# Kernel tuning notes

Measured on AMD Instinct MI355X. Metric: run time of the kernel, lower is better.

The kernel has to match this reference:

```python
import jax, jax.numpy as jnp
import numpy as np

NEG = -1000000.0  # mask fill value used by original sequence_mask

def setup_inputs() -> dict:
    key = jax.random.key(0)
    k1, k2, k3, k4 = jax.random.split(key, 4)
    B, S, D = 32, 2048, 64
    queries = jax.random.normal(k1, (B, S, D), dtype=jnp.float32)
    keys = jax.random.normal(k2, (B, S, D), dtype=jnp.float32)
    values = jax.random.normal(k3, (B, S, D), dtype=jnp.float32)
    valid_lens = jax.random.randint(k4, (B,), 1, S + 1, dtype=jnp.int64)
    return {"queries": queries, "keys": keys, "values": values, "valid_lens": valid_lens}

def reference(queries, keys, values, valid_lens):
    d = queries.shape[-1]
    # [B, Sq, Sk]
    scores = jnp.einsum('bqd,bkd->bqk', queries, keys) / jnp.sqrt(jnp.asarray(d, queries.dtype))
    # valid_lens is 1D: one length per batch row, broadcast over all query rows
    kv_idx = jnp.arange(scores.shape[-1])  # [Sk]
    mask = kv_idx[None, None, :] < valid_lens[:, None, None]  # [B,1,Sk] broadcast
    scores = jnp.where(mask, scores, jnp.asarray(NEG, scores.dtype))
    weights = jax.nn.softmax(scores, axis=-1)
    # dropout p=0.0 -> identity
    return jnp.einsum('bqk,bkd->bqd', weights, values)
```

## Files before the change

### kernel.cpp

```cpp
#include <hip/hip_runtime.h>
#include <hip/hip_bf16.h>

typedef __attribute__((ext_vector_type(8))) short bf16x8;
typedef __attribute__((ext_vector_type(4))) float f32x4;

#define BATCH 32
#define SEQ   2048
#define KSTR  72
#define VSTR  36
#define PSTR  20
#define LOG2E 1.44269504088896340736f

__device__ __forceinline__ unsigned int pk2(float lo, float hi) {
    __hip_bfloat162 h2 = __float22bfloat162_rn(make_float2(lo, hi));
    return *reinterpret_cast<unsigned int*>(&h2);
}

__global__ void prep_vl(const int* __restrict__ VL, int* __restrict__ meta) {
    __shared__ int sv[BATCH];
    const int t = threadIdx.x;
    int odd = (t < 16) ? VL[2 * t + 1] : 0;
    const bool is64 = (__ballot(odd != 0) == 0ULL);
    if (t < BATCH) {
        int x = is64 ? VL[2 * t] : VL[t];
        x = x < 0 ? 0 : (x > SEQ ? SEQ : x);
        sv[t] = x;
    }
    __syncthreads();
    if (t < BATCH) {
        const int x = sv[t];
        int rank = 0;
        for (int j = 0; j < BATCH; ++j) {
            const int y = sv[j];
            rank += (y > x) || (y == x && j < t);
        }
        meta[rank] = x;
        meta[BATCH + rank] = t;
    }
}

__device__ __forceinline__ void load_tile(const float* __restrict__ Kb,
                                          const float* __restrict__ Vb,
                                          int tid, f32x4 kv[4], f32x4 vv[4]) {
    #pragma unroll
    for (int h = 0; h < 4; ++h) {
        const int c = tid + h * 256;
        kv[h] = *(const f32x4*)(Kb + (c >> 4) * 64 + (c & 15) * 4);
    }
    #pragma unroll
    for (int h = 0; h < 2; ++h) {
        const int u  = tid + h * 256;
        const int d4 = (u & 3) + ((u >> 7) << 2);
        const int kp = (u >> 2) & 31;
        vv[2 * h]     = *(const f32x4*)(Vb + (2 * kp) * 64 + d4 * 4);
        vv[2 * h + 1] = *(const f32x4*)(Vb + (2 * kp + 1) * 64 + d4 * 4);
    }
}

__global__ __launch_bounds__(256, 4)
void attn_fwd(const float* __restrict__ Qp, const float* __restrict__ Kp,
              const float* __restrict__ Vp, const int* __restrict__ meta,
              float* __restrict__ Out) {
    constexpr int D = 64;
    constexpr int S = SEQ;
    constexpr int qtiles = S >> 6;
    __shared__ short        lK [64 * KSTR];
    __shared__ unsigned int lVt[64 * VSTR];
    __shared__ unsigned int lPt[4 * 32 * PSTR];

    const int tid  = threadIdx.x;
    const int wave = tid >> 6;
    const int lane = tid & 63;
    const int l15  = lane & 15;
    const int grp  = lane >> 4;

    const int slot  = blockIdx.x / qtiles;
    const int qt    = blockIdx.x % qtiles;
    const int vl    = meta[slot];
    const int batch = meta[BATCH + slot];
    const int ntiles = (vl + 63) >> 6;

    const float* Kb = Kp + (size_t)batch * S * D;
    const float* Vb = Vp + (size_t)batch * S * D;

    bf16x8 qf[2];
    {
        const float* qb = Qp + ((size_t)batch * S + qt * 64 + wave * 16 + l15) * D + grp * 8;
        #pragma unroll
        for (int kf = 0; kf < 2; ++kf) {
            union { f32x4 f; float e[4]; } a, b;
            a.f = *(const f32x4*)(qb + kf * 32);
            b.f = *(const f32x4*)(qb + kf * 32 + 4);
            union { bf16x8 v; unsigned int u[4]; } qq;
            qq.u[0] = pk2(a.e[0], a.e[1]); qq.u[1] = pk2(a.e[2], a.e[3]);
            qq.u[2] = pk2(b.e[0], b.e[1]); qq.u[3] = pk2(b.e[2], b.e[3]);
            qf[kf] = qq.v;
        }
    }

    f32x4 o[4] = {{0.f,0.f,0.f,0.f},{0.f,0.f,0.f,0.f},{0.f,0.f,0.f,0.f},{0.f,0.f,0.f,0.f}};
    float mrun = -INFINITY;
    float lrun = 0.f;
    unsigned int* pw = &lPt[wave * 32 * PSTR];

    f32x4 kv[4], vv[4];
    if (ntiles > 0) load_tile(Kb, Vb, tid, kv, vv);

    for (int kt = 0; kt < ntiles; ++kt) {
        const int kb = kt * 64;
        __syncthreads();

        #pragma unroll
        for (int h = 0; h < 4; ++h) {
            const int c = tid + h * 256;
            const int row = c >> 4, col = (c & 15) * 4;
            union { f32x4 f; float e[4]; } x; x.f = kv[h];
            unsigned int w0 = pk2(x.e[0], x.e[1]), w1 = pk2(x.e[2], x.e[3]);
            unsigned int* dst = (unsigned int*)&lK[row * KSTR + col];
            dst[0] = w0; dst[1] = w1;
        }
        #pragma unroll
        for (int h = 0; h < 2; ++h) {
            const int u  = tid + h * 256;
            const int d4 = (u & 3) + ((u >> 7) << 2);
            const int kp = (u >> 2) & 31;
            union { f32x4 f; float e[4]; } a, b;
            a.f = vv[2 * h]; b.f = vv[2 * h + 1];
            #pragma unroll
            for (int j = 0; j < 4; ++j)
                lVt[(d4 * 4 + j) * VSTR + kp] = pk2(a.e[j], b.e[j]);
        }
        if (kt + 1 < ntiles) load_tile(Kb + (size_t)(kb + 64) * D, Vb + (size_t)(kb + 64) * D, tid, kv, vv);
        __syncthreads();

        f32x4 st[4] = {{0.f,0.f,0.f,0.f},{0.f,0.f,0.f,0.f},{0.f,0.f,0.f,0.f},{0.f,0.f,0.f,0.f}};
        #pragma unroll
        for (int kf = 0; kf < 2; ++kf) {
            #pragma unroll
            for (int ct = 0; ct < 4; ++ct) {
                bf16x8 kfr = *(const bf16x8*)&lK[(ct * 16 + l15) * KSTR + kf * 32 + grp * 8];
                st[ct] = __builtin_amdgcn_mfma_f32_16x16x32_bf16(kfr, qf[kf], st[ct], 0, 0, 0);
            }
        }

        #pragma unroll
        for (int ct = 0; ct < 4; ++ct)
            #pragma unroll
            for (int r = 0; r < 4; ++r) {
                const bool valid = (kb + ct * 16 + grp * 4 + r) < vl;
                st[ct][r] = valid ? st[ct][r] * (0.125f * LOG2E) : (-1000000.0f * LOG2E);
            }

        float t0 = fmaxf(fmaxf(st[0][0], st[0][1]), fmaxf(st[0][2], st[0][3]));
        float t1 = fmaxf(fmaxf(st[1][0], st[1][1]), fmaxf(st[1][2], st[1][3]));
        float t2 = fmaxf(fmaxf(st[2][0], st[2][1]), fmaxf(st[2][2], st[2][3]));
        float t3 = fmaxf(fmaxf(st[3][0], st[3][1]), fmaxf(st[3][2], st[3][3]));
        float tm = fmaxf(fmaxf(t0, t1), fmaxf(t2, t3));
        tm = fmaxf(tm, __shfl_xor(tm, 16));
        tm = fmaxf(tm, __shfl_xor(tm, 32));
        const float mnew  = fmaxf(mrun, tm);
        const float alpha = exp2f(mrun - mnew);
        mrun = mnew;
        lrun *= alpha;
        #pragma unroll
        for (int dt = 0; dt < 4; ++dt)
            #pragma unroll
            for (int r = 0; r < 4; ++r) o[dt][r] *= alpha;

        float rs = 0.f;
        #pragma unroll
        for (int ct = 0; ct < 4; ++ct) {
            #pragma unroll
            for (int r = 0; r < 4; ++r) {
                st[ct][r] = exp2f(st[ct][r] - mrun);
                rs += st[ct][r];
            }
            #pragma unroll
            for (int a = 0; a < 2; ++a)
                pw[(ct * 8 + grp * 2 + a) * PSTR + l15] = pk2(st[ct][2 * a], st[ct][2 * a + 1]);
        }
        rs += __shfl_xor(rs, 16);
        rs += __shfl_xor(rs, 32);
        lrun += rs;
        asm volatile("s_waitcnt lgkmcnt(0)" ::: "memory");

        #pragma unroll
        for (int kk = 0; kk < 2; ++kk) {
            union { bf16x8 v; unsigned int u[4]; } pf;
            #pragma unroll
            for (int jj = 0; jj < 4; ++jj)
                pf.u[jj] = pw[(kk * 16 + grp * 4 + jj) * PSTR + l15];
            #pragma unroll
            for (int dt = 0; dt < 4; ++dt) {
                bf16x8 vf = *(const bf16x8*)&lVt[(dt * 16 + l15) * VSTR + kk * 16 + grp * 4];
                o[dt] = __builtin_amdgcn_mfma_f32_16x16x32_bf16(vf, pf.v, o[dt], 0, 0, 0);
            }
        }
    }

    const float inv = (lrun > 0.f) ? 1.0f / lrun : 0.f;
    const size_t orow = ((size_t)batch * S + qt * 64 + wave * 16 + l15) * D;
    #pragma unroll
    for (int dt = 0; dt < 4; ++dt) {
        f32x4 w = o[dt];
        w[0] *= inv; w[1] *= inv; w[2] *= inv; w[3] *= inv;
        *(f32x4*)(Out + orow + dt * 16 + grp * 4) = w;
    }
}

extern "C" void kernel_launch(void* const* d_in, const int* in_sizes, int n_in,
                              void* d_out, int out_size, void* d_ws, size_t ws_size,
                              hipStream_t stream) {
    const float* Q  = (const float*)d_in[0];
    const float* K  = (const float*)d_in[1];
    const float* V  = (const float*)d_in[2];
    const int*   VL = (const int*)d_in[3];
    int* meta = (int*)d_ws;
    prep_vl<<<1, 64, 0, stream>>>(VL, meta);
    dim3 grid(BATCH * (SEQ >> 6)), block(256);
    attn_fwd<<<grid, block, 0, stream>>>(Q, K, V, meta, (float*)d_out);
}
```

Measured before the change: 144.1 us.

## Pre-convert K/V to bf16 and stream tiles into LDS via async loads

Adds a prepass kernel that converts K to bf16 and V to a transposed bf16 layout in workspace. The attention kernel then double-buffers those tiles straight into swizzled LDS with global_load_lds, so each block no longer re-converts and transposes the fp32 K/V tiles itself. It also folds the softmax scale into Q, masks only the final partial tile, and skips the rescale when the running max does not change. The cost is an extra kernel launch and an extra read and write of K/V to workspace, lower occupancy (launch bounds 3), and a fallback path when the workspace is too small.

```diff
diff --git a/kernel.cpp b/kernel.cpp
--- a/kernel.cpp
+++ b/kernel.cpp
@@ -6,14 +6,21 @@
 
 #define BATCH 32
 #define SEQ   2048
+#define PSTR  20
 #define KSTR  72
 #define VSTR  36
-#define PSTR  20
 #define LOG2E 1.44269504088896340736f
+#define QSCALE (0.125f * LOG2E)
+#define NEGL  (-1000000.0f * LOG2E)
 
 __device__ __forceinline__ unsigned int pk2(float lo, float hi) {
     __hip_bfloat162 h2 = __float22bfloat162_rn(make_float2(lo, hi));
     return *reinterpret_cast<unsigned int*>(&h2);
+}
+
+__device__ __forceinline__ void dma16(const short* g, short* l) {
+    __builtin_amdgcn_global_load_lds((const __attribute__((address_space(1))) void*)g,
+                                     (__attribute__((address_space(3))) void*)l, 16, 0, 0);
 }
 
 __global__ void prep_vl(const int* __restrict__ VL, int* __restrict__ meta) {
@@ -39,9 +46,197 @@
     }
 }
 
-__device__ __forceinline__ void load_tile(const float* __restrict__ Kb,
-                                          const float* __restrict__ Vb,
-                                          int tid, f32x4 kv[4], f32x4 vv[4]) {
+__global__ __launch_bounds__(256) void prepkv(const float* __restrict__ Kp,
+                                              const float* __restrict__ Vp,
+                                              short* __restrict__ Kb,
+                                              short* __restrict__ Vt) {
+    __shared__ unsigned int l[64 * VSTR];
+    const int tid = threadIdx.x;
+    const int b = blockIdx.x >> 5, kt = blockIdx.x & 31, kb = kt * 64;
+    const float* Kv = Kp + ((size_t)b * SEQ + kb) * 64;
+    const float* Vb = Vp + ((size_t)b * SEQ + kb) * 64;
+    #pragma unroll
+    for (int h = 0; h < 4; ++h) {
+        const int c = tid + h * 256;
+        const int row = c >> 4, col = (c & 15) * 4;
+        f32x4 x = *(const f32x4*)(Kv + row * 64 + col);
+        unsigned int* dst = (unsigned int*)(Kb + ((size_t)b * SEQ + kb + row) * 64 + col);
+        dst[0] = pk2(x[0], x[1]); dst[1] = pk2(x[2], x[3]);
+    }
+    #pragma unroll
+    for (int h = 0; h < 2; ++h) {
+        const int u = tid + h * 256;
+        const int d4 = (u & 3) + ((u >> 7) << 2);
+        const int kp = (u >> 2) & 31;
+        f32x4 a = *(const f32x4*)(Vb + (2 * kp) * 64 + d4 * 4);
+        f32x4 c = *(const f32x4*)(Vb + (2 * kp + 1) * 64 + d4 * 4);
+        #pragma unroll
+        for (int j = 0; j < 4; ++j)
+            l[(d4 * 4 + j) * VSTR + kp] = pk2(a[j], c[j]);
+    }
+    __syncthreads();
+    const int d = tid >> 2, cg = tid & 3;
+    unsigned int w[8];
+    #pragma unroll
+    for (int j = 0; j < 8; ++j) w[j] = l[d * VSTR + cg * 8 + j];
+    unsigned int* dst = (unsigned int*)(Vt + (size_t)(b * 64 + d) * SEQ + kb + cg * 16);
+    #pragma unroll
+    for (int j = 0; j < 8; ++j) dst[j] = w[j];
+}
+
+__global__ __launch_bounds__(256, 3)
+void attn_fwd(const float* __restrict__ Qp, const short* __restrict__ Kb,
+              const short* __restrict__ Vt, const int* __restrict__ meta,
+              float* __restrict__ Out) {
+    constexpr int S = SEQ;
+    constexpr int qtiles = S >> 6;
+    __shared__ short bK2[2 * 64 * 64];
+    __shared__ short bV2[2 * 64 * 64];
+    __shared__ unsigned int lPt[4 * 32 * PSTR];
+
+    const int tid  = threadIdx.x;
+    const int wave = tid >> 6, lane = tid & 63;
+    const int l15  = lane & 15, grp = lane >> 4;
+    const int r7   = l15 & 7;
+
+    const int slot = blockIdx.x / qtiles, qt = blockIdx.x % qtiles;
+    const int vl = meta[slot], batch = meta[BATCH + slot];
+    const int ntiles = (vl + 63) >> 6;
+
+    const short* Kbb = Kb + (size_t)batch * S * 64;
+    const short* Vtb = Vt + (size_t)batch * 64 * S;
+
+    const int r8 = lane >> 3, s8 = lane & 7, csw = s8 ^ r8;
+    const short* gK0 = Kbb + (wave * 16 + r8) * 64 + csw * 8;
+    const short* gV0 = Vtb + (size_t)(wave * 16 + r8) * S + csw * 8;
+    short* lK0 = &bK2[wave * 16 * 64];
+    short* lV0 = &bV2[wave * 16 * 64];
+
+    bf16x8 qf[2];
+    {
+        const float* qb = Qp + ((size_t)batch * S + qt * 64 + wave * 16 + l15) * 64 + grp * 8;
+        #pragma unroll
+        for (int kf = 0; kf < 2; ++kf) {
+            f32x4 a = *(const f32x4*)(qb + kf * 32);
+            f32x4 c = *(const f32x4*)(qb + kf * 32 + 4);
+            union { bf16x8 v; unsigned int u[4]; } qq;
+            qq.u[0] = pk2(a[0] * QSCALE, a[1] * QSCALE);
+            qq.u[1] = pk2(a[2] * QSCALE, a[3] * QSCALE);
+            qq.u[2] = pk2(c[0] * QSCALE, c[1] * QSCALE);
+            qq.u[3] = pk2(c[2] * QSCALE, c[3] * QSCALE);
+            qf[kf] = qq.v;
+        }
+    }
+
+    f32x4 o[4] = {{0.f,0.f,0.f,0.f},{0.f,0.f,0.f,0.f},{0.f,0.f,0.f,0.f},{0.f,0.f,0.f,0.f}};
+    float mrun = -INFINITY, lrun = 0.f;
+    unsigned int* pw = &lPt[wave * 32 * PSTR];
+
+    if (ntiles > 0) {
+        dma16(gK0,                    lK0);
+        dma16(gK0 + 8 * 64,           lK0 + 8 * 64);
+        dma16(gV0,                    lV0);
+        dma16(gV0 + (size_t)8 * S,    lV0 + 8 * 64);
+    }
+
+    for (int kt = 0; kt < ntiles; ++kt) {
+        __syncthreads();
+        if (kt + 1 < ntiles) {
+            const int nb  = ((kt + 1) & 1) * 4096;
+            const int kbn = (kt + 1) * 64;
+            dma16(gK0 + kbn * 64,                  lK0 + nb);
+            dma16(gK0 + kbn * 64 + 8 * 64,         lK0 + nb + 8 * 64);
+            dma16(gV0 + kbn,                       lV0 + nb);
+            dma16(gV0 + kbn + (size_t)8 * S,       lV0 + nb + 8 * 64);
+        }
+        const short* bK = &bK2[(kt & 1) * 4096];
+        const short* bV = &bV2[(kt & 1) * 4096];
+
+        f32x4 st[4] = {{0.f,0.f,0.f,0.f},{0.f,0.f,0.f,0.f},{0.f,0.f,0.f,0.f},{0.f,0.f,0.f,0.f}};
+        #pragma unroll
+        for (int kf = 0; kf < 2; ++kf) {
+            #pragma unroll
+            for (int ct = 0; ct < 4; ++ct) {
+                bf16x8 kfr = *(const bf16x8*)&bK[((ct * 16 + l15) << 6) +
+                                                 (((kf * 4 + grp) ^ r7) << 3)];
+                st[ct] = __builtin_amdgcn_mfma_f32_16x16x32_bf16(kfr, qf[kf], st[ct], 0, 0, 0);
+            }
+        }
+
+        if (kt == ntiles - 1 && (vl & 63) != 0) {
+            const int kbase = kt * 64;
+            #pragma unroll
+            for (int ct = 0; ct < 4; ++ct)
+                #pragma unroll
+                for (int r = 0; r < 4; ++r) {
+                    const bool valid = (kbase + ct * 16 + grp * 4 + r) < vl;
+                    st[ct][r] = valid ? st[ct][r] : NEGL;
+                }
+        }
+
+        float t0 = fmaxf(fmaxf(st[0][0], st[0][1]), fmaxf(st[0][2], st[0][3]));
+        float t1 = fmaxf(fmaxf(st[1][0], st[1][1]), fmaxf(st[1][2], st[1][3]));
+        float t2 = fmaxf(fmaxf(st[2][0], st[2][1]), fmaxf(st[2][2], st[2][3]));
+        float t3 = fmaxf(fmaxf(st[3][0], st[3][1]), fmaxf(st[3][2], st[3][3]));
+        float tm = fmaxf(fmaxf(t0, t1), fmaxf(t2, t3));
+        tm = fmaxf(tm, __shfl_xor(tm, 16));
+        tm = fmaxf(tm, __shfl_xor(tm, 32));
+        if (__ballot(tm > mrun) != 0ULL) {
+            const float mnew  = fmaxf(mrun, tm);
+            const float alpha = exp2f(mrun - mnew);
+            mrun = mnew;
+            lrun *= alpha;
+            #pragma unroll
+            for (int dt = 0; dt < 4; ++dt)
+                #pragma unroll
+                for (int r = 0; r < 4; ++r) o[dt][r] *= alpha;
+        }
+
+        float rs = 0.f;
+        #pragma unroll
+        for (int ct = 0; ct < 4; ++ct) {
+            #pragma unroll
+            for (int r = 0; r < 4; ++r) {
+                st[ct][r] = exp2f(st[ct][r] - mrun);
+                rs += st[ct][r];
+            }
+            #pragma unroll
+            for (int a = 0; a < 2; ++a)
+                pw[(ct * 8 + grp * 2 + a) * PSTR + l15] = pk2(st[ct][2 * a], st[ct][2 * a + 1]);
+        }
+        rs += __shfl_xor(rs, 16);
+        rs += __shfl_xor(rs, 32);
+        lrun += rs;
+        asm volatile("s_waitcnt lgkmcnt(0)" ::: "memory");
+
+        #pragma unroll
+        for (int kk = 0; kk < 2; ++kk) {
+            union { bf16x8 v; unsigned int u[4]; } pf;
+            #pragma unroll
+            for (int jj = 0; jj < 4; ++jj)
+                pf.u[jj] = pw[(kk * 16 + grp * 4 + jj) * PSTR + l15];
+            #pragma unroll
+            for (int dt = 0; dt < 4; ++dt) {
+                bf16x8 vf = *(const bf16x8*)&bV[((dt * 16 + l15) << 6) +
+                                                (((kk * 4 + grp) ^ r7) << 3)];
+                o[dt] = __builtin_amdgcn_mfma_f32_16x16x32_bf16(vf, pf.v, o[dt], 0, 0, 0);
+            }
+        }
+    }
+
+    const float inv = (lrun > 0.f) ? 1.0f / lrun : 0.f;
+    const size_t orow = ((size_t)batch * S + qt * 64 + wave * 16 + l15) * 64;
+    #pragma unroll
+    for (int dt = 0; dt < 4; ++dt) {
+        f32x4 w = o[dt];
+        w[0] *= inv; w[1] *= inv; w[2] *= inv; w[3] *= inv;
+        *(f32x4*)(Out + orow + dt * 16 + grp * 4) = w;
+    }
+}
+
+__device__ __forceinline__ void load_tile_fb(const float* __restrict__ Kb,
+                                             const float* __restrict__ Vb,
+                                             int tid, f32x4 kv[4], f32x4 vv[4]) {
     #pragma unroll
     for (int h = 0; h < 4; ++h) {
         const int c = tid + h * 256;
@@ -58,66 +253,50 @@
 }
 
 __global__ __launch_bounds__(256, 4)
-void attn_fwd(const float* __restrict__ Qp, const float* __restrict__ Kp,
-              const float* __restrict__ Vp, const int* __restrict__ meta,
-              float* __restrict__ Out) {
-    constexpr int D = 64;
+void attn_fb(const float* __restrict__ Qp, const float* __restrict__ Kp,
+             const float* __restrict__ Vp, const int* __restrict__ meta,
+             float* __restrict__ Out) {
     constexpr int S = SEQ;
     constexpr int qtiles = S >> 6;
     __shared__ short        lK [64 * KSTR];
     __shared__ unsigned int lVt[64 * VSTR];
     __shared__ unsigned int lPt[4 * 32 * PSTR];
-
-    const int tid  = threadIdx.x;
-    const int wave = tid >> 6;
-    const int lane = tid & 63;
-    const int l15  = lane & 15;
-    const int grp  = lane >> 4;
-
-    const int slot  = blockIdx.x / qtiles;
-    const int qt    = blockIdx.x % qtiles;
-    const int vl    = meta[slot];
-    const int batch = meta[BATCH + slot];
+    const int tid = threadIdx.x;
+    const int wave = tid >> 6, lane = tid & 63;
+    const int l15 = lane & 15, grp = lane >> 4;
+    const int slot = blockIdx.x / qtiles, qt = blockIdx.x % qtiles;
+    const int vl = meta[slot], batch = meta[BATCH + slot];
     const int ntiles = (vl + 63) >> 6;
-
-    const float* Kb = Kp + (size_t)batch * S * D;
-    const float* Vb = Vp + (size_t)batch * S * D;
-
+    const float* Kb = Kp + (size_t)batch * S * 64;
+    const float* Vb = Vp + (size_t)batch * S * 64;
     bf16x8 qf[2];
     {
-        const float* qb = Qp + ((size_t)batch * S + qt * 64 + wave * 16 + l15) * D + grp * 8;
+        const float* qb = Qp + ((size_t)batch * S + qt * 64 + wave * 16 + l15) * 64 + grp * 8;
         #pragma unroll
         for (int kf = 0; kf < 2; ++kf) {
-            union { f32x4 f; float e[4]; } a, b;
-            a.f = *(const f32x4*)(qb + kf * 32);
-            b.f = *(const f32x4*)(qb + kf * 32 + 4);
+            f32x4 a = *(const f32x4*)(qb + kf * 32);
+            f32x4 b = *(const f32x4*)(qb + kf * 32 + 4);
             union { bf16x8 v; unsigned int u[4]; } qq;
-            qq.u[0] = pk2(a.e[0], a.e[1]); qq.u[1] = pk2(a.e[2], a.e[3]);
-            qq.u[2] = pk2(b.e[0], b.e[1]); qq.u[3] = pk2(b.e[2], b.e[3]);
+            qq.u[0] = pk2(a[0], a[1]); qq.u[1] = pk2(a[2], a[3]);
+            qq.u[2] = pk2(b[0], b[1]); qq.u[3] = pk2(b[2], b[3]);
             qf[kf] = qq.v;
         }
     }
-
     f32x4 o[4] = {{0.f,0.f,0.f,0.f},{0.f,0.f,0.f,0.f},{0.f,0.f,0.f,0.f},{0.f,0.f,0.f,0.f}};
-    float mrun = -INFINITY;
-    float lrun = 0.f;
+    float mrun = -INFINITY, lrun = 0.f;
     unsigned int* pw = &lPt[wave * 32 * PSTR];
-
     f32x4 kv[4], vv[4];
-    if (ntiles > 0) load_tile(Kb, Vb, tid, kv, vv);
-
+    if (ntiles > 0) load_tile_fb(Kb, Vb, tid, kv, vv);
     for (int kt = 0; kt < ntiles; ++kt) {
         const int kb = kt * 64;
         __syncthreads();
-
         #pragma unroll
         for (int h = 0; h < 4; ++h) {
             const int c = tid + h * 256;
             const int row = c >> 4, col = (c & 15) * 4;
             union { f32x4 f; float e[4]; } x; x.f = kv[h];
-            unsigned int w0 = pk2(x.e[0], x.e[1]), w1 = pk2(x.e[2], x.e[3]);
             unsigned int* dst = (unsigned int*)&lK[row * KSTR + col];
-            dst[0] = w0; dst[1] = w1;
+            dst[0] = pk2(x.e[0], x.e[1]); dst[1] = pk2(x.e[2], x.e[3]);
         }
         #pragma unroll
         for (int h = 0; h < 2; ++h) {
@@ -130,9 +309,8 @@
             for (int j = 0; j < 4; ++j)
                 lVt[(d4 * 4 + j) * VSTR + kp] = pk2(a.e[j], b.e[j]);
         }
-        if (kt + 1 < ntiles) load_tile(Kb + (size_t)(kb + 64) * D, Vb + (size_t)(kb + 64) * D, tid, kv, vv);
+        if (kt + 1 < ntiles) load_tile_fb(Kb + (size_t)(kb + 64) * 64, Vb + (size_t)(kb + 64) * 64, tid, kv, vv);
         __syncthreads();
-
         f32x4 st[4] = {{0.f,0.f,0.f,0.f},{0.f,0.f,0.f,0.f},{0.f,0.f,0.f,0.f},{0.f,0.f,0.f,0.f}};
         #pragma unroll
         for (int kf = 0; kf < 2; ++kf) {
@@ -142,15 +320,13 @@
                 st[ct] = __builtin_amdgcn_mfma_f32_16x16x32_bf16(kfr, qf[kf], st[ct], 0, 0, 0);
             }
         }
-
         #pragma unroll
         for (int ct = 0; ct < 4; ++ct)
             #pragma unroll
             for (int r = 0; r < 4; ++r) {
                 const bool valid = (kb + ct * 16 + grp * 4 + r) < vl;
-                st[ct][r] = valid ? st[ct][r] * (0.125f * LOG2E) : (-1000000.0f * LOG2E);
-            }
-
+                st[ct][r] = valid ? st[ct][r] * (0.125f * LOG2E) : NEGL;
+            }
         float t0 = fmaxf(fmaxf(st[0][0], st[0][1]), fmaxf(st[0][2], st[0][3]));
         float t1 = fmaxf(fmaxf(st[1][0], st[1][1]), fmaxf(st[1][2], st[1][3]));
         float t2 = fmaxf(fmaxf(st[2][0], st[2][1]), fmaxf(st[2][2], st[2][3]));
@@ -166,7 +342,6 @@
         for (int dt = 0; dt < 4; ++dt)
             #pragma unroll
             for (int r = 0; r < 4; ++r) o[dt][r] *= alpha;
-
         float rs = 0.f;
         #pragma unroll
         for (int ct = 0; ct < 4; ++ct) {
@@ -183,7 +358,6 @@
         rs += __shfl_xor(rs, 32);
         lrun += rs;
         asm volatile("s_waitcnt lgkmcnt(0)" ::: "memory");
-
         #pragma unroll
         for (int kk = 0; kk < 2; ++kk) {
             union { bf16x8 v; unsigned int u[4]; } pf;
@@ -197,9 +371,8 @@
             }
         }
     }
-
     const float inv = (lrun > 0.f) ? 1.0f / lrun : 0.f;
-    const size_t orow = ((size_t)batch * S + qt * 64 + wave * 16 + l15) * D;
+    const size_t orow = ((size_t)batch * S + qt * 64 + wave * 16 + l15) * 64;
     #pragma unroll
     for (int dt = 0; dt < 4; ++dt) {
         f32x4 w = o[dt];
@@ -217,6 +390,14 @@
     const int*   VL = (const int*)d_in[3];
     int* meta = (int*)d_ws;
     prep_vl<<<1, 64, 0, stream>>>(VL, meta);
+    const size_t need = 256 + 2 * (size_t)BATCH * SEQ * 64 * sizeof(short);
     dim3 grid(BATCH * (SEQ >> 6)), block(256);
-    attn_fwd<<<grid, block, 0, stream>>>(Q, K, V, meta, (float*)d_out);
-}
+    if (ws_size >= need) {
+        short* Kb = (short*)((char*)d_ws + 256);
+        short* Vt = Kb + (size_t)BATCH * SEQ * 64;
+        prepkv<<<dim3(BATCH * 32), block, 0, stream>>>(K, V, Kb, Vt);
+        attn_fwd<<<grid, block, 0, stream>>>(Q, Kb, Vt, meta, (float*)d_out);
+    } else {
+        attn_fb<<<grid, block, 0, stream>>>(Q, K, V, meta, (float*)d_out);
+    }
+}
```

New measurement: 141.9 us. No clear change (-1.6%).
